# Kernel optimization log

Hardware: AMD Instinct MI355X
Metric: run time of the kernel (lower is better)

## Reference

```python
import jax, jax.numpy as jnp
import numpy as np

K = 2  # num_experts_used (top-k)


def setup_inputs() -> dict:
    key = jax.random.key(0)
    ks = jax.random.split(key, 6)
    B, S, D, U, E = 2, 2048, 1024, 4096, 8
    return {
        "x": jax.random.normal(ks[0], (B, S, D), dtype=jnp.float32),
        "w_router": jax.random.normal(ks[1], (E, D), dtype=jnp.float32),
        "w_up": jax.random.normal(ks[2], (E, U, D), dtype=jnp.float32),
        "b_up": jax.random.normal(ks[3], (E, U), dtype=jnp.float32),
        "w_down": jax.random.normal(ks[4], (E, D, U), dtype=jnp.float32),
        "b_down": jax.random.normal(ks[5], (E, D), dtype=jnp.float32),
    }


def reference(x, w_router, w_up, b_up, w_down, b_down):
    # Router: Linear(embed_dim -> num_experts), no bias
    logits = jnp.einsum('bsd,ed->bse', x, w_router)
    top_logits, idx = jax.lax.top_k(logits, K)          # [b,s,k]
    router_weights = jax.nn.softmax(top_logits, axis=-1)  # softmax over top-k logits

    # Compute all-expert FFN outputs (same math as per-token gathered weights,
    # without materializing the (b,s,k,u,d) weight copies of the original).
    h = jnp.einsum('eud,bsd->bseu', w_up, x) + b_up[None, None]   # [b,s,E,u]
    h = jax.nn.gelu(h, approximate=False)
    y = jnp.einsum('edu,bseu->bsed', w_down, h) + b_down[None, None]  # [b,s,E,d]

    # Gather outputs of the top-k experts per token
    y_k = jnp.take_along_axis(y, idx[..., None], axis=2)  # [b,s,k,d]
    out = jnp.einsum('bskd,bsk->bsd', y_k, router_weights)
    return out
```

## Files before the change

kernel.cpp:

```cpp
#include <hip/hip_runtime.h>
#include <hip/hip_bf16.h>
#include <stdint.h>
#include <math.h>

#define TTOK 4096
#define DDIM 1024
#define UDIM 4096
#define NEXP 8
#define KSPLIT 2
#define KCH   (UDIM / KSPLIT)
#define NPAIR (TTOK * 2)
#define EPAD 72
#define CPAD 32
#define RBLK 128
#define CBLK 2048

using float4v = __attribute__((ext_vector_type(4))) float;
using short8  = __attribute__((ext_vector_type(8))) short;
using ushort8 = __attribute__((ext_vector_type(8))) unsigned short;
using ushort4v = __attribute__((ext_vector_type(4))) unsigned short;

__device__ __forceinline__ unsigned short f2bf(float f) {
  union { float f; unsigned u; } v; v.f = f;
  unsigned r = v.u + 0x7FFFu + ((v.u >> 16) & 1u);
  return (unsigned short)(r >> 16);
}
__device__ __forceinline__ float bf2f(unsigned short u) {
  union { unsigned u; float f; } v; v.u = ((unsigned)u) << 16;
  return v.f;
}
__device__ __forceinline__ void load_lds16(const void* g, void* l) {
  __builtin_amdgcn_global_load_lds(
      (const __attribute__((address_space(1))) unsigned int*)g,
      (__attribute__((address_space(3))) unsigned int*)l, 16, 0, 0);
}
__device__ __forceinline__ short8 cvt8(const float4v a, const float4v b) {
  union { __hip_bfloat162 h[4]; short8 s; } u;
  u.h[0] = __float22bfloat162_rn(make_float2(a[0], a[1]));
  u.h[1] = __float22bfloat162_rn(make_float2(a[2], a[3]));
  u.h[2] = __float22bfloat162_rn(make_float2(b[0], b[1]));
  u.h[3] = __float22bfloat162_rn(make_float2(b[2], b[3]));
  return u.s;
}
__device__ __forceinline__ float gelu_f(float v) {
  float u = v * (0.7978845608f + 0.0356774081f * v * v);
  float ex = __expf(2.0f * u);
  return v * (1.0f - 1.0f / (1.0f + ex));
}

__global__ void router_kernel(const float* __restrict__ x,
                              const float* __restrict__ wr,
                              int* __restrict__ counts, int* __restrict__ list,
                              float* __restrict__ wpair, int* __restrict__ epair,
                              unsigned short* __restrict__ xb) {
  const int t = blockIdx.x * 4 + (threadIdx.x >> 6);
  const int lane = threadIdx.x & 63;
  float acc[NEXP];
#pragma unroll
  for (int e = 0; e < NEXP; e++) acc[e] = 0.0f;
  const float* xr = x + (size_t)t * DDIM;
  unsigned short* xbr = xb + (size_t)t * DDIM;
  for (int d = lane; d < DDIM; d += 64) {
    float xv = xr[d];
    xbr[d] = f2bf(xv);
#pragma unroll
    for (int e = 0; e < NEXP; e++) acc[e] += xv * wr[e * DDIM + d];
  }
#pragma unroll
  for (int e = 0; e < NEXP; e++) {
#pragma unroll
    for (int off = 32; off > 0; off >>= 1) acc[e] += __shfl_xor(acc[e], off, 64);
  }
  if (lane == 0) {
    int e0 = 0; float l0 = acc[0];
    for (int e = 1; e < NEXP; e++) if (acc[e] > l0) { l0 = acc[e]; e0 = e; }
    int e1 = -1; float l1 = -3.4e38f;
    for (int e = 0; e < NEXP; e++) if (e != e0 && acc[e] > l1) { l1 = acc[e]; e1 = e; }
    float s1 = expf(l1 - l0);
    float inv = 1.0f / (1.0f + s1);
    int p0 = atomicAdd(&counts[e0 * CPAD], 1);
    list[e0 * TTOK + p0] = 2 * t;
    wpair[2 * t] = inv;  epair[2 * t] = e0;
    int p1 = atomicAdd(&counts[e1 * CPAD], 1);
    list[e1 * TTOK + p1] = 2 * t + 1;
    wpair[2 * t + 1] = s1 * inv;  epair[2 * t + 1] = e1;
  }
}

__global__ void prep_kernel(const float* __restrict__ x, const float* __restrict__ wr,
                            int* __restrict__ counts, int* __restrict__ list,
                            float* __restrict__ wpair, int* __restrict__ epair,
                            unsigned short* __restrict__ xb,
                            const float* __restrict__ wu, const float* __restrict__ wd,
                            unsigned short* __restrict__ wub, unsigned short* __restrict__ wdb) {
  __shared__ int sE0[32], sE1[32];
  const int bid = blockIdx.x;
  const int tid = threadIdx.x;

  if (bid < RBLK) {
    const int wave = tid >> 6, lane = tid & 63;
#pragma unroll 1
    for (int j = 0; j < 8; j++) {
      const int slot = wave * 8 + j;
      const int t = bid * 32 + slot;
      float acc[NEXP];
#pragma unroll
      for (int e = 0; e < NEXP; e++) acc[e] = 0.0f;
      const float* xr = x + (size_t)t * DDIM;
      unsigned short* xbr = xb + (size_t)t * DDIM;
#pragma unroll
      for (int it = 0; it < 4; it++) {
        const int d = it * 256 + lane * 4;
        float4v xv = *(const float4v*)(xr + d);
        ushort4v xo;
#pragma unroll
        for (int c = 0; c < 4; c++) xo[c] = f2bf(xv[c]);
        *(ushort4v*)(xbr + d) = xo;
#pragma unroll
        for (int e = 0; e < NEXP; e++) {
          float4v wv = *(const float4v*)(wr + e * DDIM + d);
          acc[e] += xv[0] * wv[0] + xv[1] * wv[1] + xv[2] * wv[2] + xv[3] * wv[3];
        }
      }
#pragma unroll
      for (int e = 0; e < NEXP; e++) {
#pragma unroll
        for (int off = 32; off > 0; off >>= 1) acc[e] += __shfl_xor(acc[e], off, 64);
      }
      if (lane == 0) {
        int e0 = 0; float l0 = acc[0];
        for (int e = 1; e < NEXP; e++) if (acc[e] > l0) { l0 = acc[e]; e0 = e; }
        int e1 = -1; float l1 = -3.4e38f;
        for (int e = 0; e < NEXP; e++) if (e != e0 && acc[e] > l1) { l1 = acc[e]; e1 = e; }
        float s1 = expf(l1 - l0);
        float inv = 1.0f / (1.0f + s1);
        wpair[2 * t] = inv;          epair[2 * t] = e0;
        wpair[2 * t + 1] = s1 * inv; epair[2 * t + 1] = e1;
        sE0[slot] = e0;  sE1[slot] = e1;
      }
    }
    __syncthreads();
    if (tid < NEXP) {
      const int e = tid;
      int cnt = 0;
#pragma unroll
      for (int s = 0; s < 32; s++) cnt += (sE0[s] == e) + (sE1[s] == e);
      int r = atomicAdd(&counts[e * CPAD], cnt);
      int* le = list + e * TTOK;
#pragma unroll 1
      for (int s = 0; s < 32; s++) {
        const int p = 2 * (bid * 32 + s);
        if (sE0[s] == e) le[r++] = p;
        if (sE1[s] == e) le[r++] = p + 1;
      }
    }
    return;
  }

  const int cb = bid - RBLK;
  const float* s; unsigned short* d;
  size_t i0;
  if (cb < CBLK / 2) { s = wu; d = wub; i0 = (size_t)cb * 4096; }
  else               { s = wd; d = wdb; i0 = (size_t)(cb - CBLK / 2) * 4096; }
#pragma unroll
  for (int it = 0; it < 16; it++) {
    const size_t i = i0 + (size_t)it * 256 + tid;
    float4v lo = *(const float4v*)(s + i * 8);
    float4v hi = *(const float4v*)(s + i * 8 + 4);
    *(short8*)(d + i * 8) = cvt8(lo, hi);
  }
}

__global__ __launch_bounds__(256, 4) void stage_up_b16(
    const unsigned short* __restrict__ xb, const unsigned short* __restrict__ wub,
    const float* __restrict__ bup, const int* __restrict__ counts,
    const int* __restrict__ list, unsigned short* __restrict__ h) {
  const int e = blockIdx.z, mt = blockIdx.y, nt = blockIdx.x;
  const int cnt = counts[e * CPAD];
  if (mt * 128 >= cnt) return;
  const int rem = min(128, cnt - mt * 128);
  const int* lst = list + e * TTOK + mt * 128;

  __shared__ __align__(16) char SM[18432];
  unsigned short* Sb = (unsigned short*)SM;

  const int tid = threadIdx.x;
  const int wave = tid >> 6, lane = tid & 63;
  const int srow = tid >> 2, cell = tid & 3;

  const int tok0 = lst[min(srow, rem - 1)] >> 1;
  const int tok1 = lst[min(srow + 64, rem - 1)] >> 1;
  const unsigned short* a0 = xb + (size_t)tok0 * DDIM + cell * 8;
  const unsigned short* a1 = xb + (size_t)tok1 * DDIM + cell * 8;
  const unsigned short* b0 = wub + ((size_t)e * UDIM + nt * 128 + srow) * DDIM + cell * 8;
  const unsigned short* b1 = b0 + (size_t)64 * DDIM;

  const int wm = wave >> 1, wn = wave & 1;
  const int lane15 = lane & 15, quad = lane >> 4;
  const int abyte = (wm * 64 + lane15) * 64 + quad * 16;
  const int bbyte = 8192 + (wn * 64 + lane15) * 64 + quad * 16;

  float4v acc[4][4];
#pragma unroll
  for (int i = 0; i < 4; i++)
#pragma unroll
    for (int j = 0; j < 4; j++) acc[i][j] = (float4v){0.f, 0.f, 0.f, 0.f};

  for (int k0 = 0; k0 < DDIM; k0 += 32) {
    load_lds16(a0 + k0, SM + tid * 16);
    load_lds16(a1 + k0, SM + 4096 + tid * 16);
    load_lds16(b0 + k0, SM + 8192 + tid * 16);
    load_lds16(b1 + k0, SM + 12288 + tid * 16);
    __syncthreads();
    short8 af[4], bfr[4];
#pragma unroll
    for (int mi = 0; mi < 4; mi++) af[mi] = *(const short8*)(SM + abyte + mi * 1024);
#pragma unroll
    for (int ni = 0; ni < 4; ni++) bfr[ni] = *(const short8*)(SM + bbyte + ni * 1024);
#pragma unroll
    for (int mi = 0; mi < 4; mi++)
#pragma unroll
      for (int ni = 0; ni < 4; ni++)
        acc[mi][ni] = __builtin_amdgcn_mfma_f32_16x16x32_bf16(af[mi], bfr[ni], acc[mi][ni], 0, 0, 0);
    __syncthreads();
  }

  const int ucol0 = nt * 128 + wn * 64;
  float bias[4];
#pragma unroll
  for (int ni = 0; ni < 4; ni++) bias[ni] = bup[e * UDIM + ucol0 + ni * 16 + lane15];
  const int row = tid >> 1, seg = tid & 1;
  const int opair = (row < rem) ? lst[row] : -1;
#pragma unroll
  for (int hh = 0; hh < 2; hh++) {
    if (wn == hh) {
#pragma unroll
      for (int mi = 0; mi < 4; mi++)
#pragma unroll
        for (int r = 0; r < 4; r++) {
          const int rl = wm * 64 + mi * 16 + quad * 4 + r;
#pragma unroll
          for (int ni = 0; ni < 4; ni++)
            Sb[rl * EPAD + ni * 16 + lane15] = f2bf(gelu_f(acc[mi][ni][r] + bias[ni]));
        }
    }
    __syncthreads();
    if (opair >= 0) {
      unsigned short* dst = h + (size_t)opair * UDIM + nt * 128 + hh * 64 + seg * 32;
      const unsigned short* src = Sb + row * EPAD + seg * 32;
#pragma unroll
      for (int c = 0; c < 4; c++) *(ushort8*)(dst + c * 8) = *(const ushort8*)(src + c * 8);
    }
    __syncthreads();
  }
}

__global__ __launch_bounds__(256, 4) void stage_down_b16(
    const unsigned short* __restrict__ h, const unsigned short* __restrict__ wdb,
    const int* __restrict__ counts, const int* __restrict__ list,
    unsigned short* __restrict__ part) {
  const int e = blockIdx.z, mt = blockIdx.y >> 1, kc = blockIdx.y & 1, nt = blockIdx.x;
  const int cnt = counts[e * CPAD];
  if (mt * 128 >= cnt) return;
  const int rem = min(128, cnt - mt * 128);
  const int* lst = list + e * TTOK + mt * 128;

  __shared__ __align__(16) char SM[18432];
  unsigned short* Sb = (unsigned short*)SM;

  const int tid = threadIdx.x;
  const int wave = tid >> 6, lane = tid & 63;
  const int srow = tid >> 2, cell = tid & 3;

  const int pr0 = lst[min(srow, rem - 1)];
  const int pr1 = lst[min(srow + 64, rem - 1)];
  const unsigned short* a0 = h + (size_t)pr0 * UDIM + kc * KCH + cell * 8;
  const unsigned short* a1 = h + (size_t)pr1 * UDIM + kc * KCH + cell * 8;
  const unsigned short* b0 = wdb + ((size_t)e * DDIM + nt * 128 + srow) * UDIM + kc * KCH + cell * 8;
  const unsigned short* b1 = b0 + (size_t)64 * UDIM;

  const int wm = wave >> 1, wn = wave & 1;
  const int lane15 = lane & 15, quad = lane >> 4;
  const int abyte = (wm * 64 + lane15) * 64 + quad * 16;
  const int bbyte = 8192 + (wn * 64 + lane15) * 64 + quad * 16;

  float4v acc[4][4];
#pragma unroll
  for (int i = 0; i < 4; i++)
#pragma unroll
    for (int j = 0; j < 4; j++) acc[i][j] = (float4v){0.f, 0.f, 0.f, 0.f};

  for (int k0 = 0; k0 < KCH; k0 += 32) {
    load_lds16(a0 + k0, SM + tid * 16);
    load_lds16(a1 + k0, SM + 4096 + tid * 16);
    load_lds16(b0 + k0, SM + 8192 + tid * 16);
    load_lds16(b1 + k0, SM + 12288 + tid * 16);
    __syncthreads();
    short8 af[4], bfr[4];
#pragma unroll
    for (int mi = 0; mi < 4; mi++) af[mi] = *(const short8*)(SM + abyte + mi * 1024);
#pragma unroll
    for (int ni = 0; ni < 4; ni++) bfr[ni] = *(const short8*)(SM + bbyte + ni * 1024);
#pragma unroll
    for (int mi = 0; mi < 4; mi++)
#pragma unroll
      for (int ni = 0; ni < 4; ni++)
        acc[mi][ni] = __builtin_amdgcn_mfma_f32_16x16x32_bf16(af[mi], bfr[ni], acc[mi][ni], 0, 0, 0);
    __syncthreads();
  }

  const int row = tid >> 1, seg = tid & 1;
  const int opair = (row < rem) ? lst[row] : -1;
#pragma unroll
  for (int hh = 0; hh < 2; hh++) {
    if (wn == hh) {
#pragma unroll
      for (int mi = 0; mi < 4; mi++)
#pragma unroll
        for (int r = 0; r < 4; r++) {
          const int rl = wm * 64 + mi * 16 + quad * 4 + r;
#pragma unroll
          for (int ni = 0; ni < 4; ni++)
            Sb[rl * EPAD + ni * 16 + lane15] = f2bf(acc[mi][ni][r]);
        }
    }
    __syncthreads();
    if (opair >= 0) {
      unsigned short* dst = part + ((size_t)kc * NPAIR + opair) * DDIM + nt * 128 + hh * 64 + seg * 32;
      const unsigned short* src = Sb + row * EPAD + seg * 32;
#pragma unroll
      for (int c = 0; c < 4; c++) *(ushort8*)(dst + c * 8) = *(const ushort8*)(src + c * 8);
    }
    __syncthreads();
  }
}

__global__ __launch_bounds__(256, 3) void stage_up_k(
    const unsigned short* __restrict__ xb, const float* __restrict__ wu,
    const float* __restrict__ bup, const int* __restrict__ counts,
    const int* __restrict__ list, unsigned short* __restrict__ h) {
  const int e = blockIdx.z, mt = blockIdx.y, nt = blockIdx.x;
  const int cnt = counts[e * CPAD];
  if (mt * 128 >= cnt) return;
  const int rem = min(128, cnt - mt * 128);
  const int* lst = list + e * TTOK + mt * 128;

  __shared__ __align__(16) char SM[24576];
  unsigned short* Sb = (unsigned short*)SM;

  const int tid = threadIdx.x;
  const int wave = tid >> 6, lane = tid & 63;
  const int srow = tid >> 2, cell = tid & 3;
  const int brow = tid >> 3;
  const int bswz = (tid & 7) ^ (brow & 7);

  const int tok0 = lst[min(srow, rem - 1)] >> 1;
  const int tok1 = lst[min(srow + 64, rem - 1)] >> 1;
  const unsigned short* a0 = xb + (size_t)tok0 * DDIM + cell * 8;
  const unsigned short* a1 = xb + (size_t)tok1 * DDIM + cell * 8;
  const float* bbase = wu + ((size_t)e * UDIM + nt * 128) * DDIM;
  const float* bsrc[4];
#pragma unroll
  for (int k = 0; k < 4; k++) bsrc[k] = bbase + (size_t)(brow + k * 32) * DDIM + bswz * 4;

  const int wm = wave >> 1, wn = wave & 1;
  const int lane15 = lane & 15, quad = lane >> 4;
  const int abyte = (wm * 64 + lane15) * 64 + quad * 16;
  const int p0 = (2 * quad) ^ (lane & 7);
  const int bbyte = 8192 + (wn * 64 + lane15) * 128;

  float4v acc[4][4];
#pragma unroll
  for (int i = 0; i < 4; i++)
#pragma unroll
    for (int j = 0; j < 4; j++) acc[i][j] = (float4v){0.f, 0.f, 0.f, 0.f};

  for (int k0 = 0; k0 < DDIM; k0 += 32) {
    load_lds16(a0 + k0, SM + tid * 16);
    load_lds16(a1 + k0, SM + 4096 + tid * 16);
#pragma unroll
    for (int k = 0; k < 4; k++) load_lds16(bsrc[k] + k0, SM + 8192 + k * 4096 + tid * 16);
    __syncthreads();
    short8 af[4], bfr[4];
#pragma unroll
    for (int mi = 0; mi < 4; mi++) af[mi] = *(const short8*)(SM + abyte + mi * 1024);
#pragma unroll
    for (int ni = 0; ni < 4; ni++) {
      const char* rb = SM + bbyte + ni * 2048;
      float4v f0 = *(const float4v*)(rb + p0 * 16);
      float4v f1 = *(const float4v*)(rb + (p0 ^ 1) * 16);
      bfr[ni] = cvt8(f0, f1);
    }
#pragma unroll
    for (int mi = 0; mi < 4; mi++)
#pragma unroll
      for (int ni = 0; ni < 4; ni++)
        acc[mi][ni] = __builtin_amdgcn_mfma_f32_16x16x32_bf16(af[mi], bfr[ni], acc[mi][ni], 0, 0, 0);
    __syncthreads();
  }

  const int ucol0 = nt * 128 + wn * 64;
  float bias[4];
#pragma unroll
  for (int ni = 0; ni < 4; ni++) bias[ni] = bup[e * UDIM + ucol0 + ni * 16 + lane15];
  const int row = tid >> 1, seg = tid & 1;
  const int opair = (row < rem) ? lst[row] : -1;
#pragma unroll
  for (int hh = 0; hh < 2; hh++) {
    if (wn == hh) {
#pragma unroll
      for (int mi = 0; mi < 4; mi++)
#pragma unroll
        for (int r = 0; r < 4; r++) {
          const int rl = wm * 64 + mi * 16 + quad * 4 + r;
#pragma unroll
          for (int ni = 0; ni < 4; ni++)
            Sb[rl * EPAD + ni * 16 + lane15] = f2bf(gelu_f(acc[mi][ni][r] + bias[ni]));
        }
    }
    __syncthreads();
    if (opair >= 0) {
      unsigned short* dst = h + (size_t)opair * UDIM + nt * 128 + hh * 64 + seg * 32;
      const unsigned short* src = Sb + row * EPAD + seg * 32;
#pragma unroll
      for (int c = 0; c < 4; c++) *(ushort8*)(dst + c * 8) = *(const ushort8*)(src + c * 8);
    }
    __syncthreads();
  }
}

template <bool PARTM>
__global__ __launch_bounds__(256, 3) void stage_down_k(
    const unsigned short* __restrict__ h, const float* __restrict__ wd,
    const float* __restrict__ bdn, const float* __restrict__ wpair,
    const int* __restrict__ counts, const int* __restrict__ list,
    unsigned short* __restrict__ part, float* __restrict__ out) {
  const int e = blockIdx.z, mt = blockIdx.y >> 1, kc = blockIdx.y & 1, nt = blockIdx.x;
  const int cnt = counts[e * CPAD];
  if (mt * 128 >= cnt) return;
  const int rem = min(128, cnt - mt * 128);
  const int* lst = list + e * TTOK + mt * 128;

  __shared__ __align__(16) char SM[24576];
  unsigned short* Sb = (unsigned short*)SM;

  const int tid = threadIdx.x;
  const int wave = tid >> 6, lane = tid & 63;
  const int srow = tid >> 2, cell = tid & 3;
  const int brow = tid >> 3;
  const int bswz = (tid & 7) ^ (brow & 7);

  const int pr0 = lst[min(srow, rem - 1)];
  const int pr1 = lst[min(srow + 64, rem - 1)];
  const unsigned short* a0 = h + (size_t)pr0 * UDIM + kc * KCH + cell * 8;
  const unsigned short* a1 = h + (size_t)pr1 * UDIM + kc * KCH + cell * 8;
  const float* bbase = wd + ((size_t)e * DDIM + nt * 128) * UDIM + kc * KCH;
  const float* bsrc[4];
#pragma unroll
  for (int k = 0; k < 4; k++) bsrc[k] = bbase + (size_t)(brow + k * 32) * UDIM + bswz * 4;

  const int wm = wave >> 1, wn = wave & 1;
  const int lane15 = lane & 15, quad = lane >> 4;
  const int abyte = (wm * 64 + lane15) * 64 + quad * 16;
  const int p0 = (2 * quad) ^ (lane & 7);
  const int bbyte = 8192 + (wn * 64 + lane15) * 128;

  float4v acc[4][4];
#pragma unroll
  for (int i = 0; i < 4; i++)
#pragma unroll
    for (int j = 0; j < 4; j++) acc[i][j] = (float4v){0.f, 0.f, 0.f, 0.f};

  for (int k0 = 0; k0 < KCH; k0 += 32) {
    load_lds16(a0 + k0, SM + tid * 16);
    load_lds16(a1 + k0, SM + 4096 + tid * 16);
#pragma unroll
    for (int k = 0; k < 4; k++) load_lds16(bsrc[k] + k0, SM + 8192 + k * 4096 + tid * 16);
    __syncthreads();
    short8 af[4], bfr[4];
#pragma unroll
    for (int mi = 0; mi < 4; mi++) af[mi] = *(const short8*)(SM + abyte + mi * 1024);
#pragma unroll
    for (int ni = 0; ni < 4; ni++) {
      const char* rb = SM + bbyte + ni * 2048;
      float4v f0 = *(const float4v*)(rb + p0 * 16);
      float4v f1 = *(const float4v*)(rb + (p0 ^ 1) * 16);
      bfr[ni] = cvt8(f0, f1);
    }
#pragma unroll
    for (int mi = 0; mi < 4; mi++)
#pragma unroll
      for (int ni = 0; ni < 4; ni++)
        acc[mi][ni] = __builtin_amdgcn_mfma_f32_16x16x32_bf16(af[mi], bfr[ni], acc[mi][ni], 0, 0, 0);
    __syncthreads();
  }

  const int dcol0 = nt * 128 + wn * 64;
  if constexpr (PARTM) {
    const int row = tid >> 1, seg = tid & 1;
    const int opair = (row < rem) ? lst[row] : -1;
#pragma unroll
    for (int hh = 0; hh < 2; hh++) {
      if (wn == hh) {
#pragma unroll
        for (int mi = 0; mi < 4; mi++)
#pragma unroll
          for (int r = 0; r < 4; r++) {
            const int rl = wm * 64 + mi * 16 + quad * 4 + r;
#pragma unroll
            for (int ni = 0; ni < 4; ni++)
              Sb[rl * EPAD + ni * 16 + lane15] = f2bf(acc[mi][ni][r]);
          }
      }
      __syncthreads();
      if (opair >= 0) {
        unsigned short* dst = part + ((size_t)kc * NPAIR + opair) * DDIM + nt * 128 + hh * 64 + seg * 32;
        const unsigned short* src = Sb + row * EPAD + seg * 32;
#pragma unroll
        for (int c = 0; c < 4; c++) *(ushort8*)(dst + c * 8) = *(const ushort8*)(src + c * 8);
      }
      __syncthreads();
    }
  } else {
    float bias[4];
#pragma unroll
    for (int ni = 0; ni < 4; ni++)
      bias[ni] = (kc == 0) ? bdn[e * DDIM + dcol0 + ni * 16 + lane15] : 0.0f;
#pragma unroll
    for (int mi = 0; mi < 4; mi++)
#pragma unroll
      for (int r = 0; r < 4; r++) {
        const int mrow = wm * 64 + mi * 16 + quad * 4 + r;
        if (mrow < rem) {
          const int pair = lst[mrow];
          const float w = wpair[pair];
          float* orow = out + (size_t)(pair >> 1) * DDIM;
#pragma unroll
          for (int ni = 0; ni < 4; ni++)
            atomicAdd(&orow[dcol0 + ni * 16 + lane15], w * (acc[mi][ni][r] + bias[ni]));
        }
      }
  }
}

__global__ void combine_kernel(const unsigned short* __restrict__ part,
                               const float* __restrict__ bdn,
                               const float* __restrict__ wpair,
                               const int* __restrict__ epair,
                               float* __restrict__ out) {
  const int idx = blockIdx.x * 256 + threadIdx.x;
  const int t = idx >> 7, c8 = (idx & 127) * 8;
  const size_t kstride = (size_t)NPAIR * DDIM;
  const unsigned short* pa = part + (size_t)(2 * t) * DDIM + c8;
  float s0[8], s1[8];
#pragma unroll
  for (int j = 0; j < 8; j++) { s0[j] = 0.f; s1[j] = 0.f; }
#pragma unroll
  for (int kc = 0; kc < KSPLIT; kc++) {
    ushort8 a = *(const ushort8*)(pa + kc * kstride);
    ushort8 b = *(const ushort8*)(pa + kc * kstride + DDIM);
#pragma unroll
    for (int j = 0; j < 8; j++) { s0[j] += bf2f(a[j]); s1[j] += bf2f(b[j]); }
  }
  const float w0 = wpair[2 * t], w1 = wpair[2 * t + 1];
  const int e0 = epair[2 * t], e1 = epair[2 * t + 1];
  const float* b0 = bdn + e0 * DDIM + c8;
  const float* b1 = bdn + e1 * DDIM + c8;
  float4v o[2];
#pragma unroll
  for (int half = 0; half < 2; half++)
#pragma unroll
    for (int j = 0; j < 4; j++) {
      const int jj = half * 4 + j;
      o[half][j] = w0 * (s0[jj] + b0[jj]) + w1 * (s1[jj] + b1[jj]);
    }
  float4v* dst = (float4v*)(out + (size_t)t * DDIM + c8);
  dst[0] = o[0]; dst[1] = o[1];
}

__global__ void zero_out_k(float4v* __restrict__ out) {
  const int tid = blockIdx.x * blockDim.x + threadIdx.x;
  const int O4 = TTOK * DDIM / 4;
  const int stride = gridDim.x * blockDim.x;
  for (int i = tid; i < O4; i += stride) out[i] = (float4v){0.f, 0.f, 0.f, 0.f};
}

extern "C" void kernel_launch(void* const* d_in, const int* in_sizes, int n_in,
                              void* d_out, int out_size, void* d_ws, size_t ws_size,
                              hipStream_t stream) {
  (void)in_sizes; (void)n_in; (void)out_size;
  const float* x        = (const float*)d_in[0];
  const float* w_router = (const float*)d_in[1];
  const float* w_up     = (const float*)d_in[2];
  const float* b_up     = (const float*)d_in[3];
  const float* w_down   = (const float*)d_in[4];
  const float* b_down   = (const float*)d_in[5];
  float* out = (float*)d_out;

  char* ws = (char*)d_ws;
  size_t off = 0;
  auto take = [&](size_t b) { size_t o = off; off = (off + b + 255) & ~(size_t)255; return o; };
  unsigned short* h  = (unsigned short*)(ws + take((size_t)NPAIR * UDIM * 2));
  unsigned short* xb = (unsigned short*)(ws + take((size_t)TTOK * DDIM * 2));
  int* counts        = (int*)(ws + take(NEXP * CPAD * 4));
  int* list          = (int*)(ws + take((size_t)NEXP * TTOK * 4));
  float* wpair       = (float*)(ws + take((size_t)NPAIR * 4));
  int* epair         = (int*)(ws + take((size_t)NPAIR * 4));
  size_t part_off    = take((size_t)KSPLIT * NPAIR * DDIM * 2);
  const bool partmode = ws_size >= off;
  size_t wub_off     = take((size_t)NEXP * UDIM * DDIM * 2);
  size_t wdb_off     = take((size_t)NEXP * DDIM * UDIM * 2);
  const bool bf16mode = ws_size >= off;

  hipMemsetAsync(counts, 0, NEXP * CPAD * 4, stream);

  if (bf16mode) {
    unsigned short* part = (unsigned short*)(ws + part_off);
    unsigned short* wub  = (unsigned short*)(ws + wub_off);
    unsigned short* wdb  = (unsigned short*)(ws + wdb_off);
    prep_kernel<<<RBLK + CBLK, 256, 0, stream>>>(
        x, w_router, counts, list, wpair, epair, xb, w_up, w_down, wub, wdb);
    stage_up_b16<<<dim3(UDIM / 128, 32, NEXP), 256, 0, stream>>>(
        xb, wub, b_up, counts, list, h);
    stage_down_b16<<<dim3(DDIM / 128, 32 * KSPLIT, NEXP), 256, 0, stream>>>(
        h, wdb, counts, list, part);
    combine_kernel<<<TTOK * DDIM / 8 / 256, 256, 0, stream>>>(part, b_down, wpair, epair, out);
  } else {
    router_kernel<<<TTOK / 4, 256, 0, stream>>>(x, w_router, counts, list, wpair, epair, xb);
    stage_up_k<<<dim3(UDIM / 128, 32, NEXP), 256, 0, stream>>>(xb, w_up, b_up, counts, list, h);
    if (partmode) {
      unsigned short* part = (unsigned short*)(ws + part_off);
      stage_down_k<true><<<dim3(DDIM / 128, 32 * KSPLIT, NEXP), 256, 0, stream>>>(
          h, w_down, b_down, wpair, counts, list, part, out);
      combine_kernel<<<TTOK * DDIM / 8 / 256, 256, 0, stream>>>(part, b_down, wpair, epair, out);
    } else {
      zero_out_k<<<1024, 256, 0, stream>>>((float4v*)out);
      stage_down_k<false><<<dim3(DDIM / 128, 32 * KSPLIT, NEXP), 256, 0, stream>>>(
          h, w_down, b_down, wpair, counts, list, (unsigned short*)nullptr, out);
    }
  }
}
```

Before: 602.9 us.

## Overlap w_down bf16 conversion with up-projection via idle-block ticket queue

The prep kernel now converts only w_up to bf16. The w_down conversion moves into stage_up_b16: blocks whose expert row tile is empty grab chunks from an atomic ticket counter and convert them, so the work overlaps the up GEMM instead of running serially beforehand. Weight conversion now uses nontemporal loads and stores to avoid polluting cache. The down-stage grid is also reordered so that m-tiles and k-splits vary fastest. This relies on there being enough idle blocks, and the ticket loop adds atomics, but correctness holds because every chunk is claimed.

```diff
diff --git a/kernel.cpp b/kernel.cpp
--- a/kernel.cpp
+++ b/kernel.cpp
@@ -13,7 +13,7 @@
 #define EPAD 72
 #define CPAD 32
 #define RBLK 128
-#define CBLK 2048
+#define WCHUNK 2048
 
 using float4v = __attribute__((ext_vector_type(4))) float;
 using short8  = __attribute__((ext_vector_type(8))) short;
@@ -33,6 +33,12 @@
   __builtin_amdgcn_global_load_lds(
       (const __attribute__((address_space(1))) unsigned int*)g,
       (__attribute__((address_space(3))) unsigned int*)l, 16, 0, 0);
+}
+__device__ __forceinline__ float4v ntld4(const float* p) {
+  return __builtin_nontemporal_load((const float4v*)p);
+}
+__device__ __forceinline__ void ntst8(unsigned short* p, const short8 v) {
+  __builtin_nontemporal_store(v, (short8*)p);
 }
 __device__ __forceinline__ short8 cvt8(const float4v a, const float4v b) {
   union { __hip_bfloat162 h[4]; short8 s; } u;
@@ -91,8 +97,8 @@
                             int* __restrict__ counts, int* __restrict__ list,
                             float* __restrict__ wpair, int* __restrict__ epair,
                             unsigned short* __restrict__ xb,
-                            const float* __restrict__ wu, const float* __restrict__ wd,
-                            unsigned short* __restrict__ wub, unsigned short* __restrict__ wdb) {
+                            const float* __restrict__ wu,
+                            unsigned short* __restrict__ wub) {
   __shared__ int sE0[32], sE1[32];
   const int bid = blockIdx.x;
   const int tid = threadIdx.x;
@@ -157,34 +163,51 @@
     return;
   }
 
-  const int cb = bid - RBLK;
-  const float* s; unsigned short* d;
-  size_t i0;
-  if (cb < CBLK / 2) { s = wu; d = wub; i0 = (size_t)cb * 4096; }
-  else               { s = wd; d = wdb; i0 = (size_t)(cb - CBLK / 2) * 4096; }
-#pragma unroll
-  for (int it = 0; it < 16; it++) {
-    const size_t i = i0 + (size_t)it * 256 + tid;
-    float4v lo = *(const float4v*)(s + i * 8);
-    float4v hi = *(const float4v*)(s + i * 8 + 4);
-    *(short8*)(d + i * 8) = cvt8(lo, hi);
+  const size_t g0 = (size_t)(bid - RBLK) * 2048;
+#pragma unroll
+  for (int it = 0; it < 8; it++) {
+    const size_t i = g0 + it * 256 + tid;
+    float4v lo = ntld4(wu + i * 8);
+    float4v hi = ntld4(wu + i * 8 + 4);
+    ntst8(wub + i * 8, cvt8(lo, hi));
   }
 }
 
 __global__ __launch_bounds__(256, 4) void stage_up_b16(
     const unsigned short* __restrict__ xb, const unsigned short* __restrict__ wub,
     const float* __restrict__ bup, const int* __restrict__ counts,
-    const int* __restrict__ list, unsigned short* __restrict__ h) {
+    const int* __restrict__ list, unsigned short* __restrict__ h,
+    const float* __restrict__ wd, unsigned short* __restrict__ wdb,
+    int* __restrict__ ticket) {
   const int e = blockIdx.z, mt = blockIdx.y, nt = blockIdx.x;
   const int cnt = counts[e * CPAD];
-  if (mt * 128 >= cnt) return;
+
+  __shared__ __align__(16) char SM[18432];
+  unsigned short* Sb = (unsigned short*)SM;
+  const int tid = threadIdx.x;
+
+  if (mt * 128 >= cnt) {
+    int* sc = (int*)SM;
+    for (;;) {
+      if (tid == 0) *sc = atomicAdd(ticket, 1);
+      __syncthreads();
+      const int c = *sc;
+      __syncthreads();
+      if (c >= WCHUNK) return;
+      const size_t g0 = (size_t)c * 2048;
+#pragma unroll
+      for (int it = 0; it < 8; it++) {
+        const size_t i = g0 + it * 256 + tid;
+        float4v lo = ntld4(wd + i * 8);
+        float4v hi = ntld4(wd + i * 8 + 4);
+        ntst8(wdb + i * 8, cvt8(lo, hi));
+      }
+    }
+  }
+
   const int rem = min(128, cnt - mt * 128);
   const int* lst = list + e * TTOK + mt * 128;
 
-  __shared__ __align__(16) char SM[18432];
-  unsigned short* Sb = (unsigned short*)SM;
-
-  const int tid = threadIdx.x;
   const int wave = tid >> 6, lane = tid & 63;
   const int srow = tid >> 2, cell = tid & 3;
 
@@ -259,7 +282,7 @@
     const unsigned short* __restrict__ h, const unsigned short* __restrict__ wdb,
     const int* __restrict__ counts, const int* __restrict__ list,
     unsigned short* __restrict__ part) {
-  const int e = blockIdx.z, mt = blockIdx.y >> 1, kc = blockIdx.y & 1, nt = blockIdx.x;
+  const int e = blockIdx.z, mt = blockIdx.x >> 1, kc = blockIdx.x & 1, nt = blockIdx.y;
   const int cnt = counts[e * CPAD];
   if (mt * 128 >= cnt) return;
   const int rem = min(128, cnt - mt * 128);
@@ -602,7 +625,8 @@
   auto take = [&](size_t b) { size_t o = off; off = (off + b + 255) & ~(size_t)255; return o; };
   unsigned short* h  = (unsigned short*)(ws + take((size_t)NPAIR * UDIM * 2));
   unsigned short* xb = (unsigned short*)(ws + take((size_t)TTOK * DDIM * 2));
-  int* counts        = (int*)(ws + take(NEXP * CPAD * 4));
+  int* counts        = (int*)(ws + take((NEXP * CPAD + 64) * 4));
+  int* ticket        = counts + NEXP * CPAD;
   int* list          = (int*)(ws + take((size_t)NEXP * TTOK * 4));
   float* wpair       = (float*)(ws + take((size_t)NPAIR * 4));
   int* epair         = (int*)(ws + take((size_t)NPAIR * 4));
@@ -612,17 +636,17 @@
   size_t wdb_off     = take((size_t)NEXP * DDIM * UDIM * 2);
   const bool bf16mode = ws_size >= off;
 
-  hipMemsetAsync(counts, 0, NEXP * CPAD * 4, stream);
+  hipMemsetAsync(counts, 0, (NEXP * CPAD + 64) * 4, stream);
 
   if (bf16mode) {
     unsigned short* part = (unsigned short*)(ws + part_off);
     unsigned short* wub  = (unsigned short*)(ws + wub_off);
     unsigned short* wdb  = (unsigned short*)(ws + wdb_off);
-    prep_kernel<<<RBLK + CBLK, 256, 0, stream>>>(
-        x, w_router, counts, list, wpair, epair, xb, w_up, w_down, wub, wdb);
+    prep_kernel<<<RBLK + WCHUNK, 256, 0, stream>>>(
+        x, w_router, counts, list, wpair, epair, xb, w_up, wub);
     stage_up_b16<<<dim3(UDIM / 128, 32, NEXP), 256, 0, stream>>>(
-        xb, wub, b_up, counts, list, h);
-    stage_down_b16<<<dim3(DDIM / 128, 32 * KSPLIT, NEXP), 256, 0, stream>>>(
+        xb, wub, b_up, counts, list, h, w_down, wdb, ticket);
+    stage_down_b16<<<dim3(32 * KSPLIT, DDIM / 128, NEXP), 256, 0, stream>>>(
         h, wdb, counts, list, part);
     combine_kernel<<<TTOK * DDIM / 8 / 256, 256, 0, stream>>>(part, b_down, wpair, epair, out);
   } else {
```

After: 632.4 us. 1.05x slower.
